# Optimization experiments

Measured on AMD Instinct MI355X. Metric: run time of the kernel, lower is better.

The kernel has to match this reference:

```python
import jax, jax.numpy as jnp
import numpy as np
from jax import lax

PS = 8  # patch size

def setup_inputs() -> dict:
    key = jax.random.key(0)
    ks = jax.random.split(key, 7)
    dim = 64
    B, H, W = 4, 256, 256
    x = jax.random.normal(ks[0], (B, dim, H, W), dtype=jnp.float32)
    # to_hidden: Conv2d(dim, 6*dim, k=1)
    w_hidden = jax.random.normal(ks[1], (6 * dim, dim, 1, 1), dtype=jnp.float32) * 0.05
    b_hidden = jax.random.normal(ks[2], (6 * dim,), dtype=jnp.float32) * 0.01
    # to_hidden_dw: depthwise Conv2d(6*dim, 6*dim, k=3, pad=1, groups=6*dim)
    w_dw = jax.random.normal(ks[3], (6 * dim, 1, 3, 3), dtype=jnp.float32) * 0.05
    b_dw = jax.random.normal(ks[4], (6 * dim,), dtype=jnp.float32) * 0.01
    # project_out: Conv2d(2*dim, dim, k=1)
    w_out = jax.random.normal(ks[5], (dim, 2 * dim, 1, 1), dtype=jnp.float32) * 0.05
    b_out = jax.random.normal(ks[6], (dim,), dtype=jnp.float32) * 0.01
    return {"x": x, "w_hidden": w_hidden, "b_hidden": b_hidden,
            "w_dw": w_dw, "b_dw": b_dw, "w_out": w_out, "b_out": b_out}

def _conv(x, w, groups=1, padding='VALID'):
    return lax.conv_general_dilated(
        x, w, window_strides=(1, 1), padding=padding,
        dimension_numbers=('NCHW', 'OIHW', 'NCHW'),
        feature_group_count=groups)

def reference(x, w_hidden, b_hidden, w_dw, b_dw, w_out, b_out):
    # 1x1 expansion to 6*dim channels
    hidden = _conv(x, w_hidden) + b_hidden[None, :, None, None]
    # 3x3 depthwise conv (groups == channels)
    dw = _conv(hidden, w_dw, groups=w_dw.shape[0], padding='SAME') + b_dw[None, :, None, None]
    q, k, v = jnp.split(dw, 3, axis=1)  # each (B, 2*dim, H, W)
    B, C, H, W = q.shape
    # raw reshape into (B,C,H/8,W/8,8,8) exactly as torch .reshape on contiguous NCHW
    q_patch = q.reshape(B, C, H // PS, W // PS, PS, PS)
    k_patch = k.reshape(B, C, H // PS, W // PS, PS, PS)
    q_fft = jnp.fft.rfft2(q_patch)
    k_fft = jnp.fft.rfft2(k_patch)
    out = jnp.fft.irfft2(q_fft * k_fft, s=(PS, PS))  # circular conv of q,k patches
    out = out.reshape(B, C, (H // PS) * PS, (W // PS) * PS)
    output = v * out
    output = _conv(output, w_out) + b_out[None, :, None, None]
    return output
```

## Files before the change

### kernel.cpp

```cpp
#include <hip/hip_runtime.h>

#define HW 65536
#define W_IMG 256
#define H_IMG 256
#define CIN 64
#define CHID 384
#define CQK 128

__global__ __launch_bounds__(256) void k1_expand(
    const float* __restrict__ x_base,
    const float* __restrict__ wh,
    const float* __restrict__ bh,
    float* __restrict__ hidden_base,
    size_t x_bstride, size_t hid_bstride)
{
    const float* x = x_base + blockIdx.z * x_bstride;
    float* hidden  = hidden_base + blockIdx.z * hid_bstride;
    const int pxbase = blockIdx.x * 256;
    const int cobase = blockIdx.y * 48;
    const int tid  = threadIdx.x;
    const int lane = tid & 63;
    const int wq   = __builtin_amdgcn_readfirstlane(tid >> 6);
    const int px   = pxbase + lane * 4;
    const int cw   = cobase + wq * 12;

    float acc[12][4];
    #pragma unroll
    for (int i = 0; i < 12; ++i)
        #pragma unroll
        for (int j = 0; j < 4; ++j) acc[i][j] = 0.f;

    float4 xa[4], xb[4];
    #pragma unroll
    for (int u = 0; u < 4; ++u)
        xa[u] = *reinterpret_cast<const float4*>(&x[(size_t)u * HW + px]);

    #pragma unroll 1
    for (int ci4 = 0; ci4 < CIN; ci4 += 8) {
        #pragma unroll
        for (int u = 0; u < 4; ++u)
            xb[u] = *reinterpret_cast<const float4*>(&x[(size_t)(ci4 + 4 + u) * HW + px]);
        #pragma unroll
        for (int i = 0; i < 12; ++i) {
            float4 wv = *reinterpret_cast<const float4*>(
                &wh[(size_t)(cw + i) * CIN + ci4]);
            float wu[4] = {wv.x, wv.y, wv.z, wv.w};
            #pragma unroll
            for (int u = 0; u < 4; ++u) {
                acc[i][0] += wu[u] * xa[u].x;
                acc[i][1] += wu[u] * xa[u].y;
                acc[i][2] += wu[u] * xa[u].z;
                acc[i][3] += wu[u] * xa[u].w;
            }
        }
        if (ci4 + 8 < CIN) {
            #pragma unroll
            for (int u = 0; u < 4; ++u)
                xa[u] = *reinterpret_cast<const float4*>(&x[(size_t)(ci4 + 8 + u) * HW + px]);
        }
        #pragma unroll
        for (int i = 0; i < 12; ++i) {
            float4 wv = *reinterpret_cast<const float4*>(
                &wh[(size_t)(cw + i) * CIN + ci4 + 4]);
            float wu[4] = {wv.x, wv.y, wv.z, wv.w};
            #pragma unroll
            for (int u = 0; u < 4; ++u) {
                acc[i][0] += wu[u] * xb[u].x;
                acc[i][1] += wu[u] * xb[u].y;
                acc[i][2] += wu[u] * xb[u].z;
                acc[i][3] += wu[u] * xb[u].w;
            }
        }
    }

    #pragma unroll
    for (int i = 0; i < 12; ++i) {
        int co = cw + i;
        float b = bh[co];
        float4 o;
        o.x = acc[i][0] + b; o.y = acc[i][1] + b;
        o.z = acc[i][2] + b; o.w = acc[i][3] + b;
        *reinterpret_cast<float4*>(&hidden[(size_t)co * HW + px]) = o;
    }
}

#define QK_CH   2208
#define QK_ROW  276
#define QK_SEG  68
__global__ __launch_bounds__(256) void k2_fused(
    const float* __restrict__ hidden_base,
    const float* __restrict__ wdw,
    const float* __restrict__ bdw,
    float* __restrict__ vout_base,
    size_t hid_bstride, size_t vout_bstride)
{
    __shared__ float stgq[10 * 264];
    __shared__ float stgk[10 * 264];
    __shared__ float qk[2 * QK_CH];

    const float* hidden = hidden_base + blockIdx.z * hid_bstride;
    float* vout         = vout_base + blockIdx.z * vout_bstride;

    const int c  = blockIdx.y;
    const int r0 = blockIdx.x * 8;
    const int tid = threadIdx.x;

    const int row = tid >> 5;
    const int seg = (tid >> 3) & 3;
    const int i   = tid & 7;
    const int gr  = r0 + row;
    const int wp0 = seg * 64 + i * 8;

    float4 qreg[3], kreg[3];
    #pragma unroll
    for (int it = 0; it < 3; ++it) {
        int f4 = it * 256 + tid;
        qreg[it] = make_float4(0.f, 0.f, 0.f, 0.f);
        if (f4 < 640) {
            int lr = f4 >> 6, p4 = f4 & 63;
            int grr = r0 - 1 + lr;
            if ((unsigned)grr < H_IMG)
                qreg[it] = *reinterpret_cast<const float4*>(
                    &hidden[(size_t)c * HW + (size_t)grr * W_IMG + p4 * 4]);
        }
    }
    #pragma unroll
    for (int it = 0; it < 3; ++it) {
        int f4 = it * 256 + tid;
        kreg[it] = make_float4(0.f, 0.f, 0.f, 0.f);
        if (f4 < 640) {
            int lr = f4 >> 6, p4 = f4 & 63;
            int grr = r0 - 1 + lr;
            if ((unsigned)grr < H_IMG)
                kreg[it] = *reinterpret_cast<const float4*>(
                    &hidden[(size_t)(c + CQK) * HW + (size_t)grr * W_IMG + p4 * 4]);
        }
    }

    #pragma unroll
    for (int it = 0; it < 3; ++it) {
        int f4 = it * 256 + tid;
        if (f4 < 640) {
            int lr = f4 >> 6, p4 = f4 & 63;
            *reinterpret_cast<float4*>(&stgq[lr * 264 + 4 + p4 * 4]) = qreg[it];
            *reinterpret_cast<float4*>(&stgk[lr * 264 + 4 + p4 * 4]) = kreg[it];
        }
    }
    if (tid < 10) {
        stgq[tid * 264 + 3]   = 0.f;
        stgq[tid * 264 + 260] = 0.f;
        stgk[tid * 264 + 3]   = 0.f;
        stgk[tid * 264 + 260] = 0.f;
    }

    const float* hbv = hidden + (size_t)(c + 2 * CQK) * HW;
    float4 hv[3][2];
    float  hm[3], hp[3];
    #pragma unroll
    for (int ky = 0; ky < 3; ++ky) {
        int grr = gr + ky - 1;
        hv[ky][0] = make_float4(0.f, 0.f, 0.f, 0.f);
        hv[ky][1] = make_float4(0.f, 0.f, 0.f, 0.f);
        hm[ky] = 0.f; hp[ky] = 0.f;
        if ((unsigned)grr < H_IMG) {
            const float* rb = hbv + (size_t)grr * W_IMG;
            hv[ky][0] = *reinterpret_cast<const float4*>(&rb[wp0]);
            hv[ky][1] = *reinterpret_cast<const float4*>(&rb[wp0 + 4]);
            hm[ky] = (wp0 > 0)   ? rb[wp0 - 1] : 0.f;
            hp[ky] = (wp0 < 248) ? rb[wp0 + 8] : 0.f;
        }
    }

    __syncthreads();

    const int w = tid;
    const int segw = w >> 6;
    const int tw   = w & 63;

    #pragma unroll
    for (int ch = 0; ch < 2; ++ch) {
        const float* S = ch ? stgk : stgq;
        const float* wv = wdw + (c + ch * CQK) * 9;
        const float bias = bdw[c + ch * CQK];
        const float w0 = wv[0], w1 = wv[1], w2 = wv[2];
        const float w3 = wv[3], w4 = wv[4], w5 = wv[5];
        const float w6 = wv[6], w7 = wv[7], w8 = wv[8];

        const float* S0 = S + w + 3;
        float am = S0[0],   a0 = S0[1],   ap = S0[2];
        float bm = S0[264], b0 = S0[265], bp = S0[266];
        #pragma unroll
        for (int r = 0; r < 8; ++r) {
            const float* Sr = S0 + (r + 2) * 264;
            float cm = Sr[0], c0 = Sr[1], cp = Sr[2];
            float a = bias + am * w0 + a0 * w1 + ap * w2
                           + bm * w3 + b0 * w4 + bp * w5
                           + cm * w6 + c0 * w7 + cp * w8;
            qk[ch * QK_CH + r * QK_ROW + segw * QK_SEG + tw] = a;
            am = bm; a0 = b0; ap = bp;
            bm = cm; b0 = c0; bp = cp;
        }
    }
    __syncthreads();

    const float* qb = &qk[row * QK_ROW + seg * QK_SEG];
    const float* kb = &qk[QK_CH + row * QK_ROW + seg * QK_SEG];

    float acc[8];
    #pragma unroll
    for (int j = 0; j < 8; ++j) acc[j] = 0.f;

    #pragma unroll
    for (int s = 0; s < 8; ++s) {
        int qr = (i - s) & 7;
        float4 ka = *reinterpret_cast<const float4*>(&kb[s * 8]);
        float4 kc = *reinterpret_cast<const float4*>(&kb[s * 8 + 4]);
        float4 qa = *reinterpret_cast<const float4*>(&qb[qr * 8]);
        float4 qc = *reinterpret_cast<const float4*>(&qb[qr * 8 + 4]);
        float kr[8] = {ka.x, ka.y, ka.z, ka.w, kc.x, kc.y, kc.z, kc.w};
        float qv[8] = {qa.x, qa.y, qa.z, qa.w, qc.x, qc.y, qc.z, qc.w};
        #pragma unroll
        for (int t = 0; t < 8; ++t)
            #pragma unroll
            for (int j = 0; j < 8; ++j)
                acc[j] += kr[t] * qv[(j - t) & 7];
    }

    const float* wvv = wdw + (c + 2 * CQK) * 9;
    const float vbias = bdw[c + 2 * CQK];
    float vc[8];
    #pragma unroll
    for (int j = 0; j < 8; ++j) vc[j] = vbias;
    #pragma unroll
    for (int ky = 0; ky < 3; ++ky) {
        float kw0 = wvv[ky * 3], kw1 = wvv[ky * 3 + 1], kw2 = wvv[ky * 3 + 2];
        float h[10];
        h[0] = hm[ky];
        h[1] = hv[ky][0].x; h[2] = hv[ky][0].y; h[3] = hv[ky][0].z; h[4] = hv[ky][0].w;
        h[5] = hv[ky][1].x; h[6] = hv[ky][1].y; h[7] = hv[ky][1].z; h[8] = hv[ky][1].w;
        h[9] = hp[ky];
        #pragma unroll
        for (int j = 0; j < 8; ++j)
            vc[j] += h[j] * kw0 + h[j + 1] * kw1 + h[j + 2] * kw2;
    }

    float* dst = &vout[(size_t)c * HW + (size_t)gr * W_IMG + wp0];
    float4 o0, o1;
    o0.x = acc[0] * vc[0]; o0.y = acc[1] * vc[1];
    o0.z = acc[2] * vc[2]; o0.w = acc[3] * vc[3];
    o1.x = acc[4] * vc[4]; o1.y = acc[5] * vc[5];
    o1.z = acc[6] * vc[6]; o1.w = acc[7] * vc[7];
    *reinterpret_cast<float4*>(dst)     = o0;
    *reinterpret_cast<float4*>(dst + 4) = o1;
}

__global__ __launch_bounds__(256) void k3_project(
    const float* __restrict__ vout_base,
    const float* __restrict__ wo,
    const float* __restrict__ bo,
    float* __restrict__ out_base,
    size_t vout_bstride, size_t out_bstride)
{
    const float* vout = vout_base + blockIdx.z * vout_bstride;
    float* out        = out_base + blockIdx.z * out_bstride;
    const int pxbase = blockIdx.x * 256;
    const int cobase = blockIdx.y * 16;
    const int tid  = threadIdx.x;
    const int lane = tid & 63;
    const int wq   = __builtin_amdgcn_readfirstlane(tid >> 6);
    const int px   = pxbase + lane * 4;
    const int cw   = cobase + wq * 4;

    float acc[4][4];
    #pragma unroll
    for (int i = 0; i < 4; ++i)
        #pragma unroll
        for (int j = 0; j < 4; ++j) acc[i][j] = 0.f;

    float4 xa[4], xb[4];
    #pragma unroll
    for (int u = 0; u < 4; ++u)
        xa[u] = *reinterpret_cast<const float4*>(&vout[(size_t)u * HW + px]);

    #pragma unroll 1
    for (int cc4 = 0; cc4 < CQK; cc4 += 8) {
        #pragma unroll
        for (int u = 0; u < 4; ++u)
            xb[u] = *reinterpret_cast<const float4*>(&vout[(size_t)(cc4 + 4 + u) * HW + px]);
        #pragma unroll
        for (int i = 0; i < 4; ++i) {
            float4 wv = *reinterpret_cast<const float4*>(
                &wo[(size_t)(cw + i) * CQK + cc4]);
            float wu[4] = {wv.x, wv.y, wv.z, wv.w};
            #pragma unroll
            for (int u = 0; u < 4; ++u) {
                acc[i][0] += wu[u] * xa[u].x;
                acc[i][1] += wu[u] * xa[u].y;
                acc[i][2] += wu[u] * xa[u].z;
                acc[i][3] += wu[u] * xa[u].w;
            }
        }
        if (cc4 + 8 < CQK) {
            #pragma unroll
            for (int u = 0; u < 4; ++u)
                xa[u] = *reinterpret_cast<const float4*>(&vout[(size_t)(cc4 + 8 + u) * HW + px]);
        }
        #pragma unroll
        for (int i = 0; i < 4; ++i) {
            float4 wv = *reinterpret_cast<const float4*>(
                &wo[(size_t)(cw + i) * CQK + cc4 + 4]);
            float wu[4] = {wv.x, wv.y, wv.z, wv.w};
            #pragma unroll
            for (int u = 0; u < 4; ++u) {
                acc[i][0] += wu[u] * xb[u].x;
                acc[i][1] += wu[u] * xb[u].y;
                acc[i][2] += wu[u] * xb[u].z;
                acc[i][3] += wu[u] * xb[u].w;
            }
        }
    }

    #pragma unroll
    for (int i = 0; i < 4; ++i) {
        int co = cw + i;
        float b = bo[co];
        float4 o;
        o.x = acc[i][0] + b; o.y = acc[i][1] + b;
        o.z = acc[i][2] + b; o.w = acc[i][3] + b;
        *reinterpret_cast<float4*>(&out[(size_t)co * HW + px]) = o;
    }
}

extern "C" void kernel_launch(void* const* d_in, const int* in_sizes, int n_in,
                              void* d_out, int out_size, void* d_ws, size_t ws_size,
                              hipStream_t stream) {
    const float* x   = (const float*)d_in[0];
    const float* wh  = (const float*)d_in[1];
    const float* bh  = (const float*)d_in[2];
    const float* wdw = (const float*)d_in[3];
    const float* bdw = (const float*)d_in[4];
    const float* wo  = (const float*)d_in[5];
    const float* bo  = (const float*)d_in[6];
    float* out = (float*)d_out;

    const size_t n_hid  = (size_t)CHID * HW;
    const size_t n_vout = (size_t)CQK * HW;
    const size_t n_x    = (size_t)CIN * HW;

    if (ws_size >= 4 * (n_hid + n_vout) * sizeof(float)) {
        float* hidden = (float*)d_ws;
        float* vout   = hidden + 4 * n_hid;
        k1_expand <<<dim3(HW / 256, CHID / 48, 4), 256, 0, stream>>>(
            x, wh, bh, hidden, n_x, n_hid);
        k2_fused  <<<dim3(H_IMG / 8, CQK, 4),      256, 0, stream>>>(
            hidden, wdw, bdw, vout, n_hid, n_vout);
        k3_project<<<dim3(HW / 256, 64 / 16, 4),   256, 0, stream>>>(
            vout, wo, bo, out, n_vout, n_x);
    } else {
        float* hidden = (float*)d_ws;
        float* vout   = hidden + n_hid;
        for (int b = 0; b < 4; ++b) {
            const float* xb = x + (size_t)b * n_x;
            float* ob       = out + (size_t)b * n_x;
            k1_expand <<<dim3(HW / 256, CHID / 48, 1), 256, 0, stream>>>(
                xb, wh, bh, hidden, 0, 0);
            k2_fused  <<<dim3(H_IMG / 8, CQK, 1),      256, 0, stream>>>(
                hidden, wdw, bdw, vout, 0, 0);
            k3_project<<<dim3(HW / 256, 64 / 16, 1),   256, 0, stream>>>(
                vout, wo, bo, ob, 0, 0);
        }
    }
}
```

Baseline: 398.9 us.

## Split expand accumulators into two passes; compute q/k depthwise from registers with shuffles

The 1x1 expansion kernel now handles its 12 output channels per wave as two sequential groups of 6, halving the live accumulators and likely lowering register pressure so more waves fit, at the cost of reloading x twice. The fused depthwise kernel drops the shared-memory staging of q/k halo rows and one barrier. Each thread now loads its own 3 rows of 8 pixels directly from global memory and gets horizontal neighbours through lane shuffles. This removes LDS traffic and a sync but adds redundant global reads of halo rows across threads.

Measured after the change: 424.8 us. 6.5% more time.

```diff
diff --git a/kernel.cpp b/kernel.cpp
--- a/kernel.cpp
+++ b/kernel.cpp
@@ -22,65 +22,68 @@
     const int lane = tid & 63;
     const int wq   = __builtin_amdgcn_readfirstlane(tid >> 6);
     const int px   = pxbase + lane * 4;
-    const int cw   = cobase + wq * 12;
-
-    float acc[12][4];
-    #pragma unroll
-    for (int i = 0; i < 12; ++i)
-        #pragma unroll
-        for (int j = 0; j < 4; ++j) acc[i][j] = 0.f;
-
-    float4 xa[4], xb[4];
-    #pragma unroll
-    for (int u = 0; u < 4; ++u)
-        xa[u] = *reinterpret_cast<const float4*>(&x[(size_t)u * HW + px]);
-
-    #pragma unroll 1
-    for (int ci4 = 0; ci4 < CIN; ci4 += 8) {
+
+    #pragma unroll
+    for (int g = 0; g < 2; ++g) {
+        const int cw = cobase + g * 24 + wq * 6;
+        float acc[6][4];
+        #pragma unroll
+        for (int i = 0; i < 6; ++i)
+            #pragma unroll
+            for (int j = 0; j < 4; ++j) acc[i][j] = 0.f;
+
+        float4 xa[4], xb[4];
         #pragma unroll
         for (int u = 0; u < 4; ++u)
-            xb[u] = *reinterpret_cast<const float4*>(&x[(size_t)(ci4 + 4 + u) * HW + px]);
-        #pragma unroll
-        for (int i = 0; i < 12; ++i) {
-            float4 wv = *reinterpret_cast<const float4*>(
-                &wh[(size_t)(cw + i) * CIN + ci4]);
-            float wu[4] = {wv.x, wv.y, wv.z, wv.w};
-            #pragma unroll
-            for (int u = 0; u < 4; ++u) {
-                acc[i][0] += wu[u] * xa[u].x;
-                acc[i][1] += wu[u] * xa[u].y;
-                acc[i][2] += wu[u] * xa[u].z;
-                acc[i][3] += wu[u] * xa[u].w;
-            }
-        }
-        if (ci4 + 8 < CIN) {
+            xa[u] = *reinterpret_cast<const float4*>(&x[(size_t)u * HW + px]);
+
+        #pragma unroll 1
+        for (int ci4 = 0; ci4 < CIN; ci4 += 8) {
             #pragma unroll
             for (int u = 0; u < 4; ++u)
-                xa[u] = *reinterpret_cast<const float4*>(&x[(size_t)(ci4 + 8 + u) * HW + px]);
-        }
-        #pragma unroll
-        for (int i = 0; i < 12; ++i) {
-            float4 wv = *reinterpret_cast<const float4*>(
-                &wh[(size_t)(cw + i) * CIN + ci4 + 4]);
-            float wu[4] = {wv.x, wv.y, wv.z, wv.w};
-            #pragma unroll
-            for (int u = 0; u < 4; ++u) {
-                acc[i][0] += wu[u] * xb[u].x;
-                acc[i][1] += wu[u] * xb[u].y;
-                acc[i][2] += wu[u] * xb[u].z;
-                acc[i][3] += wu[u] * xb[u].w;
-            }
-        }
-    }
-
-    #pragma unroll
-    for (int i = 0; i < 12; ++i) {
-        int co = cw + i;
-        float b = bh[co];
-        float4 o;
-        o.x = acc[i][0] + b; o.y = acc[i][1] + b;
-        o.z = acc[i][2] + b; o.w = acc[i][3] + b;
-        *reinterpret_cast<float4*>(&hidden[(size_t)co * HW + px]) = o;
+                xb[u] = *reinterpret_cast<const float4*>(&x[(size_t)(ci4 + 4 + u) * HW + px]);
+            #pragma unroll
+            for (int i = 0; i < 6; ++i) {
+                float4 wv = *reinterpret_cast<const float4*>(
+                    &wh[(size_t)(cw + i) * CIN + ci4]);
+                float wu[4] = {wv.x, wv.y, wv.z, wv.w};
+                #pragma unroll
+                for (int u = 0; u < 4; ++u) {
+                    acc[i][0] += wu[u] * xa[u].x;
+                    acc[i][1] += wu[u] * xa[u].y;
+                    acc[i][2] += wu[u] * xa[u].z;
+                    acc[i][3] += wu[u] * xa[u].w;
+                }
+            }
+            if (ci4 + 8 < CIN) {
+                #pragma unroll
+                for (int u = 0; u < 4; ++u)
+                    xa[u] = *reinterpret_cast<const float4*>(&x[(size_t)(ci4 + 8 + u) * HW + px]);
+            }
+            #pragma unroll
+            for (int i = 0; i < 6; ++i) {
+                float4 wv = *reinterpret_cast<const float4*>(
+                    &wh[(size_t)(cw + i) * CIN + ci4 + 4]);
+                float wu[4] = {wv.x, wv.y, wv.z, wv.w};
+                #pragma unroll
+                for (int u = 0; u < 4; ++u) {
+                    acc[i][0] += wu[u] * xb[u].x;
+                    acc[i][1] += wu[u] * xb[u].y;
+                    acc[i][2] += wu[u] * xb[u].z;
+                    acc[i][3] += wu[u] * xb[u].w;
+                }
+            }
+        }
+
+        #pragma unroll
+        for (int i = 0; i < 6; ++i) {
+            int co = cw + i;
+            float b = bh[co];
+            float4 o;
+            o.x = acc[i][0] + b; o.y = acc[i][1] + b;
+            o.z = acc[i][2] + b; o.w = acc[i][3] + b;
+            *reinterpret_cast<float4*>(&hidden[(size_t)co * HW + px]) = o;
+        }
     }
 }
 
@@ -94,8 +97,6 @@
     float* __restrict__ vout_base,
     size_t hid_bstride, size_t vout_bstride)
 {
-    __shared__ float stgq[10 * 264];
-    __shared__ float stgk[10 * 264];
     __shared__ float qk[2 * QK_CH];
 
     const float* hidden = hidden_base + blockIdx.z * hid_bstride;
@@ -105,62 +106,73 @@
     const int r0 = blockIdx.x * 8;
     const int tid = threadIdx.x;
 
-    const int row = tid >> 5;
+    const int row   = tid >> 5;
+    const int col32 = tid & 31;
+    const int px8   = col32 * 8;
+    const int gro   = r0 + row;
+
+    float4 qa0[3], qa1[3], ka0[3], ka1[3];
+    #pragma unroll
+    for (int ky = 0; ky < 3; ++ky) {
+        int grr = gro + ky - 1;
+        qa0[ky] = make_float4(0.f,0.f,0.f,0.f); qa1[ky] = qa0[ky];
+        ka0[ky] = qa0[ky];                      ka1[ky] = qa0[ky];
+        if ((unsigned)grr < H_IMG) {
+            const float* rq = hidden + (size_t)c * HW + (size_t)grr * W_IMG;
+            const float* rk = hidden + (size_t)(c + CQK) * HW + (size_t)grr * W_IMG;
+            qa0[ky] = *reinterpret_cast<const float4*>(&rq[px8]);
+            qa1[ky] = *reinterpret_cast<const float4*>(&rq[px8 + 4]);
+            ka0[ky] = *reinterpret_cast<const float4*>(&rk[px8]);
+            ka1[ky] = *reinterpret_cast<const float4*>(&rk[px8 + 4]);
+        }
+    }
+
+    #pragma unroll
+    for (int ch = 0; ch < 2; ++ch) {
+        const float4* a0 = ch ? ka0 : qa0;
+        const float4* a1 = ch ? ka1 : qa1;
+        const float* wv = wdw + (c + ch * CQK) * 9;
+        const float bias = bdw[c + ch * CQK];
+
+        float accd[8];
+        #pragma unroll
+        for (int j = 0; j < 8; ++j) accd[j] = bias;
+
+        #pragma unroll
+        for (int ky = 0; ky < 3; ++ky) {
+            float kw0 = wv[ky * 3], kw1 = wv[ky * 3 + 1], kw2 = wv[ky * 3 + 2];
+            float lf = __shfl_up(a1[ky].w, 1);
+            float rt = __shfl_down(a0[ky].x, 1);
+            if (col32 == 0)  lf = 0.f;
+            if (col32 == 31) rt = 0.f;
+            float h[10] = {lf, a0[ky].x, a0[ky].y, a0[ky].z, a0[ky].w,
+                               a1[ky].x, a1[ky].y, a1[ky].z, a1[ky].w, rt};
+            #pragma unroll
+            for (int j = 0; j < 8; ++j)
+                accd[j] += h[j] * kw0 + h[j + 1] * kw1 + h[j + 2] * kw2;
+        }
+
+        float* dst = &qk[ch * QK_CH + row * QK_ROW + (px8 >> 6) * QK_SEG + (px8 & 63)];
+        float4 o0, o1;
+        o0.x = accd[0]; o0.y = accd[1]; o0.z = accd[2]; o0.w = accd[3];
+        o1.x = accd[4]; o1.y = accd[5]; o1.z = accd[6]; o1.w = accd[7];
+        *reinterpret_cast<float4*>(dst)     = o0;
+        *reinterpret_cast<float4*>(dst + 4) = o1;
+    }
+
     const int seg = (tid >> 3) & 3;
     const int i   = tid & 7;
     const int gr  = r0 + row;
     const int wp0 = seg * 64 + i * 8;
 
-    float4 qreg[3], kreg[3];
-    #pragma unroll
-    for (int it = 0; it < 3; ++it) {
-        int f4 = it * 256 + tid;
-        qreg[it] = make_float4(0.f, 0.f, 0.f, 0.f);
-        if (f4 < 640) {
-            int lr = f4 >> 6, p4 = f4 & 63;
-            int grr = r0 - 1 + lr;
-            if ((unsigned)grr < H_IMG)
-                qreg[it] = *reinterpret_cast<const float4*>(
-                    &hidden[(size_t)c * HW + (size_t)grr * W_IMG + p4 * 4]);
-        }
-    }
-    #pragma unroll
-    for (int it = 0; it < 3; ++it) {
-        int f4 = it * 256 + tid;
-        kreg[it] = make_float4(0.f, 0.f, 0.f, 0.f);
-        if (f4 < 640) {
-            int lr = f4 >> 6, p4 = f4 & 63;
-            int grr = r0 - 1 + lr;
-            if ((unsigned)grr < H_IMG)
-                kreg[it] = *reinterpret_cast<const float4*>(
-                    &hidden[(size_t)(c + CQK) * HW + (size_t)grr * W_IMG + p4 * 4]);
-        }
-    }
-
-    #pragma unroll
-    for (int it = 0; it < 3; ++it) {
-        int f4 = it * 256 + tid;
-        if (f4 < 640) {
-            int lr = f4 >> 6, p4 = f4 & 63;
-            *reinterpret_cast<float4*>(&stgq[lr * 264 + 4 + p4 * 4]) = qreg[it];
-            *reinterpret_cast<float4*>(&stgk[lr * 264 + 4 + p4 * 4]) = kreg[it];
-        }
-    }
-    if (tid < 10) {
-        stgq[tid * 264 + 3]   = 0.f;
-        stgq[tid * 264 + 260] = 0.f;
-        stgk[tid * 264 + 3]   = 0.f;
-        stgk[tid * 264 + 260] = 0.f;
-    }
-
     const float* hbv = hidden + (size_t)(c + 2 * CQK) * HW;
     float4 hv[3][2];
     float  hm[3], hp[3];
     #pragma unroll
     for (int ky = 0; ky < 3; ++ky) {
         int grr = gr + ky - 1;
-        hv[ky][0] = make_float4(0.f, 0.f, 0.f, 0.f);
-        hv[ky][1] = make_float4(0.f, 0.f, 0.f, 0.f);
+        hv[ky][0] = make_float4(0.f,0.f,0.f,0.f);
+        hv[ky][1] = make_float4(0.f,0.f,0.f,0.f);
         hm[ky] = 0.f; hp[ky] = 0.f;
         if ((unsigned)grr < H_IMG) {
             const float* rb = hbv + (size_t)grr * W_IMG;
@@ -171,36 +183,6 @@
         }
     }
 
-    __syncthreads();
-
-    const int w = tid;
-    const int segw = w >> 6;
-    const int tw   = w & 63;
-
-    #pragma unroll
-    for (int ch = 0; ch < 2; ++ch) {
-        const float* S = ch ? stgk : stgq;
-        const float* wv = wdw + (c + ch * CQK) * 9;
-        const float bias = bdw[c + ch * CQK];
-        const float w0 = wv[0], w1 = wv[1], w2 = wv[2];
-        const float w3 = wv[3], w4 = wv[4], w5 = wv[5];
-        const float w6 = wv[6], w7 = wv[7], w8 = wv[8];
-
-        const float* S0 = S + w + 3;
-        float am = S0[0],   a0 = S0[1],   ap = S0[2];
-        float bm = S0[264], b0 = S0[265], bp = S0[266];
-        #pragma unroll
-        for (int r = 0; r < 8; ++r) {
-            const float* Sr = S0 + (r + 2) * 264;
-            float cm = Sr[0], c0 = Sr[1], cp = Sr[2];
-            float a = bias + am * w0 + a0 * w1 + ap * w2
-                           + bm * w3 + b0 * w4 + bp * w5
-                           + cm * w6 + c0 * w7 + cp * w8;
-            qk[ch * QK_CH + r * QK_ROW + segw * QK_SEG + tw] = a;
-            am = bm; a0 = b0; ap = bp;
-            bm = cm; b0 = c0; bp = cp;
-        }
-    }
     __syncthreads();
 
     const float* qb = &qk[row * QK_ROW + seg * QK_SEG];
```

## Process batch sequentially with per-batch workspace and nontemporal hidden stores

Applied to the files above, without the earlier changes.

Drops the batched single-launch path and always runs the three kernels once per batch image, reusing a workspace sized for one image so the hidden and vout intermediates can stay resident in the large last-level cache between kernels. The hidden tensor is written with nontemporal stores in the expansion kernel. The trade is four times as many launches, each with a smaller grid. Nontemporal stores may also push the hidden data out of cache before k2 reads it, which works against the cache-residency goal.

Result: slower. 425.1 us (+6.6%).

```diff
diff --git a/kernel.cpp b/kernel.cpp
--- a/kernel.cpp
+++ b/kernel.cpp
@@ -7,15 +7,19 @@
 #define CHID 384
 #define CQK 128
 
+typedef float nfloat4 __attribute__((ext_vector_type(4)));
+
+__device__ __forceinline__ void nt_store4(float* p, float a, float b, float c, float d) {
+    nfloat4 v; v.x = a; v.y = b; v.z = c; v.w = d;
+    __builtin_nontemporal_store(v, reinterpret_cast<nfloat4*>(p));
+}
+
 __global__ __launch_bounds__(256) void k1_expand(
-    const float* __restrict__ x_base,
+    const float* __restrict__ x,
     const float* __restrict__ wh,
     const float* __restrict__ bh,
-    float* __restrict__ hidden_base,
-    size_t x_bstride, size_t hid_bstride)
+    float* __restrict__ hidden)
 {
-    const float* x = x_base + blockIdx.z * x_bstride;
-    float* hidden  = hidden_base + blockIdx.z * hid_bstride;
     const int pxbase = blockIdx.x * 256;
     const int cobase = blockIdx.y * 48;
     const int tid  = threadIdx.x;
@@ -77,10 +81,8 @@
     for (int i = 0; i < 12; ++i) {
         int co = cw + i;
         float b = bh[co];
-        float4 o;
-        o.x = acc[i][0] + b; o.y = acc[i][1] + b;
-        o.z = acc[i][2] + b; o.w = acc[i][3] + b;
-        *reinterpret_cast<float4*>(&hidden[(size_t)co * HW + px]) = o;
+        nt_store4(&hidden[(size_t)co * HW + px],
+                  acc[i][0] + b, acc[i][1] + b, acc[i][2] + b, acc[i][3] + b);
     }
 }
 
@@ -88,18 +90,14 @@
 #define QK_ROW  276
 #define QK_SEG  68
 __global__ __launch_bounds__(256) void k2_fused(
-    const float* __restrict__ hidden_base,
+    const float* __restrict__ hidden,
     const float* __restrict__ wdw,
     const float* __restrict__ bdw,
-    float* __restrict__ vout_base,
-    size_t hid_bstride, size_t vout_bstride)
+    float* __restrict__ vout)
 {
     __shared__ float stgq[10 * 264];
     __shared__ float stgk[10 * 264];
     __shared__ float qk[2 * QK_CH];
-
-    const float* hidden = hidden_base + blockIdx.z * hid_bstride;
-    float* vout         = vout_base + blockIdx.z * vout_bstride;
 
     const int c  = blockIdx.y;
     const int r0 = blockIdx.x * 8;
@@ -255,14 +253,11 @@
 }
 
 __global__ __launch_bounds__(256) void k3_project(
-    const float* __restrict__ vout_base,
+    const float* __restrict__ vout,
     const float* __restrict__ wo,
     const float* __restrict__ bo,
-    float* __restrict__ out_base,
-    size_t vout_bstride, size_t out_bstride)
+    float* __restrict__ out)
 {
-    const float* vout = vout_base + blockIdx.z * vout_bstride;
-    float* out        = out_base + blockIdx.z * out_bstride;
     const int pxbase = blockIdx.x * 256;
     const int cobase = blockIdx.y * 16;
     const int tid  = threadIdx.x;
@@ -347,27 +342,13 @@
     const size_t n_vout = (size_t)CQK * HW;
     const size_t n_x    = (size_t)CIN * HW;
 
-    if (ws_size >= 4 * (n_hid + n_vout) * sizeof(float)) {
-        float* hidden = (float*)d_ws;
-        float* vout   = hidden + 4 * n_hid;
-        k1_expand <<<dim3(HW / 256, CHID / 48, 4), 256, 0, stream>>>(
-            x, wh, bh, hidden, n_x, n_hid);
-        k2_fused  <<<dim3(H_IMG / 8, CQK, 4),      256, 0, stream>>>(
-            hidden, wdw, bdw, vout, n_hid, n_vout);
-        k3_project<<<dim3(HW / 256, 64 / 16, 4),   256, 0, stream>>>(
-            vout, wo, bo, out, n_vout, n_x);
-    } else {
-        float* hidden = (float*)d_ws;
-        float* vout   = hidden + n_hid;
-        for (int b = 0; b < 4; ++b) {
-            const float* xb = x + (size_t)b * n_x;
-            float* ob       = out + (size_t)b * n_x;
-            k1_expand <<<dim3(HW / 256, CHID / 48, 1), 256, 0, stream>>>(
-                xb, wh, bh, hidden, 0, 0);
-            k2_fused  <<<dim3(H_IMG / 8, CQK, 1),      256, 0, stream>>>(
-                hidden, wdw, bdw, vout, 0, 0);
-            k3_project<<<dim3(HW / 256, 64 / 16, 1),   256, 0, stream>>>(
-                vout, wo, bo, ob, 0, 0);
-        }
-    }
-}
+    float* hidden = (float*)d_ws;
+    float* vout   = hidden + n_hid;
+    for (int b = 0; b < 4; ++b) {
+        const float* xb = x + (size_t)b * n_x;
+        float* ob       = out + (size_t)b * n_x;
+        k1_expand <<<dim3(HW / 256, CHID / 48), 256, 0, stream>>>(xb, wh, bh, hidden);
+        k2_fused  <<<dim3(H_IMG / 8, CQK),      256, 0, stream>>>(hidden, wdw, bdw, vout);
+        k3_project<<<dim3(HW / 256, 64 / 16),   256, 0, stream>>>(vout, wo, bo, ob);
+    }
+}
```
